# Kernel optimization log

Hardware: AMD Instinct MI355X
Metric: run time of the kernel (lower is better)

## Reference

```python
import jax, jax.numpy as jnp
import numpy as np
import math

B, D_MODEL, H, D_K, L = 24, 128, 8, 16, 512


def setup_inputs() -> dict:
    key = jax.random.key(0)
    ks = jax.random.split(key, 5)
    x = jax.random.normal(ks[0], (B, D_MODEL, L), dtype=jnp.float32)
    Wq = jax.random.normal(ks[1], (H, B, D_K, D_MODEL), dtype=jnp.float32)
    Wk = jax.random.normal(ks[2], (H, B, D_K, D_MODEL), dtype=jnp.float32)
    Wv = jax.random.normal(ks[3], (H, B, D_K, D_MODEL), dtype=jnp.float32)
    Wo = jax.random.normal(ks[4], (B, H * D_K, D_MODEL), dtype=jnp.float32)
    return {"x": x, "Wq": Wq, "Wk": Wk, "Wv": Wv, "Wo": Wo}


def reference(x, Wq, Wk, Wv, Wo):
    # Per-head, per-batch projections: [h,b,k,d] @ [b,d,l] -> [h,b,k,l]
    Q = jnp.einsum('hbkd,bdl->hbkl', Wq, x)
    K = jnp.einsum('hbkd,bdl->hbkl', Wk, x)
    V = jnp.einsum('hbkd,bdl->hbkl', Wv, x)
    # scores[h,b,l,m] = Q[:, :, :, l] . K[:, :, :, m]; torch softmax dim=1 of
    # the [B, L, L] score -> softmax over the QUERY axis l (axis=2 here).
    scores = jnp.einsum('hbkl,hbkm->hblm', Q, K) / math.sqrt(D_K)
    attn = jax.nn.softmax(scores, axis=2)
    # head_i = V @ attn : [h,b,v,l] @ [h,b,l,m] -> [h,b,v,m]
    heads = jnp.einsum('hbvl,hblm->hbvm', V, attn)
    # concat heads along channel dim: [b, h*v, L]
    head = heads.transpose(1, 0, 2, 3).reshape(B, H * D_K, L)
    # out = Wo @ head : [b, h*v, d_model] treated as [b,128,128] @ [b,128,L]
    out = jnp.einsum('bod,bdl->bol', Wo, head)
    return out
```

## Files before the change

### kernel.cpp

```cpp
#include <hip/hip_runtime.h>
#include <math.h>

#define NB 24
#define DM 128
#define NH 8
#define DK 16
#define LL 512
#define HB (NH * NB)

#define XTH_OFF 0
#define XTL_OFF 3145728
#define WHI_OFF 6291456
#define WLO_OFF 8650752
#define WOB_OFF 11010048
#define QB_OFF  11796480
#define KB_OFF  18087936
#define VB_OFF  24379392
#define HT_OFF  27525120

typedef __attribute__((ext_vector_type(8))) short bf16x8;
typedef __attribute__((ext_vector_type(4))) float f32x4;
typedef __attribute__((ext_vector_type(4))) int   i32x4;

#define MFMA  __builtin_amdgcn_mfma_f32_16x16x32_bf16
#define EXP2  __builtin_amdgcn_exp2f
#define BPERM __builtin_amdgcn_ds_bpermute

static __device__ __forceinline__ unsigned bfr(float x) {
    return (__float_as_uint(x) + 0x8000u) & 0xffff0000u;
}
static __device__ __forceinline__ unsigned pk2(unsigned e, unsigned o) {
    return (e >> 16) | o;
}

__global__ __launch_bounds__(256)
void prep(const float* __restrict__ x,
          const float* __restrict__ Wq,
          const float* __restrict__ Wk,
          const float* __restrict__ Wv,
          const float* __restrict__ Wo,
          unsigned short* __restrict__ xthi,
          unsigned short* __restrict__ xtlo,
          unsigned short* __restrict__ whi,
          unsigned short* __restrict__ wlo,
          unsigned short* __restrict__ wob)
{
    __shared__ float T[128][65];
    const int bid = blockIdx.x, tid = threadIdx.x;

    if (bid < 192) {
        const int b = bid >> 3, lc = bid & 7;
        const float* __restrict__ xb = x + (size_t)b * 65536 + lc * 64;
        #pragma unroll
        for (int i = 0; i < 32; ++i) {
            const int idx = i * 256 + tid;
            T[idx >> 6][idx & 63] = xb[(size_t)(idx >> 6) * LL + (idx & 63)];
        }
        __syncthreads();
        #pragma unroll
        for (int i = 0; i < 32; ++i) {
            const int idx = i * 256 + tid;
            const int l = idx >> 7, d = idx & 127;
            const float v = T[d][l];
            const unsigned h = bfr(v);
            const size_t o = (size_t)b * 65536 + (size_t)(lc * 64 + l) * DM + d;
            xthi[o] = (unsigned short)(h >> 16);
            xtlo[o] = (unsigned short)(bfr(v - __uint_as_float(h)) >> 16);
        }
    } else if (bid < 768) {
        const int w = bid - 192, hb = w / 3, mat = w - hb * 3;
        const float* __restrict__ src =
            (mat == 0 ? Wq : (mat == 1 ? Wk : Wv)) + (size_t)hb * 2048;
        unsigned short* __restrict__ dh = whi + (size_t)w * 2048;
        unsigned short* __restrict__ dl = wlo + (size_t)w * 2048;
        for (int i = tid; i < 2048; i += 256) {
            const float v = src[i];
            const unsigned h = bfr(v);
            dh[i] = (unsigned short)(h >> 16);
            dl[i] = (unsigned short)(bfr(v - __uint_as_float(h)) >> 16);
        }
    } else {
        const int w = bid - 768;
        const float* __restrict__ src = Wo + (size_t)w * 4096;
        unsigned short* __restrict__ d = wob + (size_t)w * 4096;
        for (int i = tid; i < 4096; i += 256)
            d[i] = (unsigned short)(bfr(src[i]) >> 16);
    }
}

__global__ __launch_bounds__(256)
void qkv_mfma(const unsigned short* __restrict__ xthi,
              const unsigned short* __restrict__ xtlo,
              const unsigned short* __restrict__ whi,
              const unsigned short* __restrict__ wlo,
              unsigned short* __restrict__ qb,
              unsigned short* __restrict__ kb,
              unsigned short* __restrict__ vb)
{
    const int blk  = blockIdx.x;
    const int nc   = blk & 1;
    const int hm   = blk >> 1;
    const int mat  = hm % 3;
    const int hb   = hm / 3;
    const int b    = hb % NB;
    const int wv   = threadIdx.x >> 6;
    const int lane = threadIdx.x & 63;
    const int g = lane >> 4, mR = lane & 15;
    const int l0 = nc * 256 + wv * 64;

    const unsigned short* __restrict__ wA = whi + (size_t)hm * 2048 + mR * 128 + g * 8;
    const unsigned short* __restrict__ wB = wlo + (size_t)hm * 2048 + mR * 128 + g * 8;
    const unsigned short* __restrict__ xh = xthi + (size_t)b * 65536 + g * 8;
    const unsigned short* __restrict__ xl = xtlo + (size_t)b * 65536 + g * 8;

    f32x4 C[4];
    #pragma unroll
    for (int t = 0; t < 4; ++t) C[t] = (f32x4){0.f, 0.f, 0.f, 0.f};

    #pragma unroll
    for (int kk = 0; kk < 4; ++kk) {
        const bf16x8 aH = *(const bf16x8*)(wA + kk * 32);
        const bf16x8 aL = *(const bf16x8*)(wB + kk * 32);
        #pragma unroll
        for (int t = 0; t < 4; ++t) {
            const size_t lo_ = (size_t)(l0 + t * 16 + mR) * DM + kk * 32;
            const bf16x8 bH = *(const bf16x8*)(xh + lo_);
            const bf16x8 bL = *(const bf16x8*)(xl + lo_);
            C[t] = MFMA(aH, bH, C[t], 0, 0, 0);
            C[t] = MFMA(aH, bL, C[t], 0, 0, 0);
            C[t] = MFMA(aL, bH, C[t], 0, 0, 0);
        }
    }

    if (mat == 2) {
        unsigned short* __restrict__ vo = vb + (size_t)hb * 8192;
        #pragma unroll
        for (int t = 0; t < 4; ++t) {
            const int l = l0 + t * 16 + mR;
            #pragma unroll
            for (int i = 0; i < 4; ++i)
                vo[(size_t)(4 * g + i) * LL + l] =
                    (unsigned short)(bfr(C[t][i]) >> 16);
        }
    } else {
        const float scale = (mat == 1) ? (0.25f * 1.44269504f) : 1.0f;
        unsigned short* __restrict__ dst =
            (mat == 0 ? qb : kb) + (size_t)hb * LL * 32;
        #pragma unroll
        for (int t = 0; t < 4; ++t) {
            const int l = l0 + t * 16 + mR;
            ushort4 hi4, lo4;
            #pragma unroll
            for (int i = 0; i < 4; ++i) {
                const float v = C[t][i] * scale;
                const unsigned h = bfr(v);
                const unsigned lw = bfr(v - __uint_as_float(h));
                ((unsigned short*)&hi4)[i] = (unsigned short)(h >> 16);
                ((unsigned short*)&lo4)[i] = (unsigned short)(lw >> 16);
            }
            *(ushort4*)(dst + (size_t)l * 32 + 4 * g)      = hi4;
            *(ushort4*)(dst + (size_t)l * 32 + 16 + 4 * g) = lo4;
        }
    }
}

static __device__ __forceinline__ void soft_pv(
    const f32x4& s0, const f32x4& s1, float tm, float& bar, float& sm,
    f32x4& O, const bf16x8& aV, int aLo, int aHi, bool up)
{
    const float nb = fmaxf(bar, tm + 32.f);
    const float f  = EXP2(bar - nb);
    bar = nb;
    const unsigned u0 = bfr(EXP2(s0[0]-nb)), u1 = bfr(EXP2(s0[1]-nb));
    const unsigned u2 = bfr(EXP2(s0[2]-nb)), u3 = bfr(EXP2(s0[3]-nb));
    const unsigned w0 = bfr(EXP2(s1[0]-nb)), w1 = bfr(EXP2(s1[1]-nb));
    const unsigned w2 = bfr(EXP2(s1[2]-nb)), w3 = bfr(EXP2(s1[3]-nb));
    const float sacc =
        ((__uint_as_float(u0) + __uint_as_float(u1)) +
         (__uint_as_float(u2) + __uint_as_float(u3))) +
        ((__uint_as_float(w0) + __uint_as_float(w1)) +
         (__uint_as_float(w2) + __uint_as_float(w3)));
    sm = fmaf(sm, f, sacc);
    O *= f;
    const int c0 = (int)pk2(u0, u1), c1 = (int)pk2(u2, u3);
    const int c2 = (int)pk2(w0, w1), c3 = (int)pk2(w2, w3);
    const int p00 = BPERM(aLo, c0), p02 = BPERM(aLo, c2);
    const int p10 = BPERM(aLo, c1), p12 = BPERM(aLo, c3);
    const int p20 = BPERM(aHi, c0), p22 = BPERM(aHi, c2);
    const int p30 = BPERM(aHi, c1), p32 = BPERM(aHi, c3);
    i32x4 bi = { up ? p00 : p02, up ? p10 : p12,
                 up ? p20 : p22, up ? p30 : p32 };
    O = MFMA(aV, __builtin_bit_cast(bf16x8, bi), O, 0, 0, 0);
}

__global__ __launch_bounds__(256)
void attn_mfma(const unsigned short* __restrict__ qb,
               const unsigned short* __restrict__ kb,
               const unsigned short* __restrict__ vb,
               unsigned short* __restrict__ ht)
{
    const int hb   = blockIdx.x >> 2;
    const int mc   = blockIdx.x & 3;
    const int tid  = threadIdx.x;
    const int wave = tid >> 6;
    const int lane = tid & 63;
    const int g    = lane >> 4;
    const int mR   = lane & 15;
    const int mb   = mc * 128 + wave * 32;

    const unsigned short* Kr0 = kb + ((size_t)hb * LL + mb + mR) * 32;
    const unsigned short* Kr1 = Kr0 + 16 * 32;
    const bf16x8 bK0  = *(const bf16x8*)(Kr0 + g * 8);
    const bf16x8 bK0s = *(const bf16x8*)(Kr0 + (g ^ 2) * 8);
    const bf16x8 bK1  = *(const bf16x8*)(Kr1 + g * 8);
    const bf16x8 bK1s = *(const bf16x8*)(Kr1 + (g ^ 2) * 8);

    const unsigned short* qrow = qb + ((size_t)hb * LL + mR) * 32 + g * 8;
    const unsigned short* vrow = vb + ((size_t)hb * DK + mR) * LL + g * 8;

    f32x4 O0 = {0.f,0.f,0.f,0.f}, O1 = {0.f,0.f,0.f,0.f};
    float bar0 = -1e30f, bar1 = -1e30f, sm0 = 0.f, sm1 = 0.f;

    const int aLo = ((g & 1) * 32 + mR) * 4;
    const int aHi = aLo + 64;
    const bool up = (g < 2);

    for (int l = 0; l < LL; l += 32) {
        const bf16x8 aQ0 = *(const bf16x8*)(qrow + (size_t)l * 32);
        const bf16x8 aQ1 = *(const bf16x8*)(qrow + (size_t)(l + 16) * 32);

        const f32x4 z = {0.f,0.f,0.f,0.f};
        f32x4 sA0 = MFMA(aQ0, bK0, z, 0,0,0);  sA0 = MFMA(aQ0, bK0s, sA0, 0,0,0);
        f32x4 sB0 = MFMA(aQ0, bK1, z, 0,0,0);  sB0 = MFMA(aQ0, bK1s, sB0, 0,0,0);
        f32x4 sA1 = MFMA(aQ1, bK0, z, 0,0,0);  sA1 = MFMA(aQ1, bK0s, sA1, 0,0,0);
        f32x4 sB1 = MFMA(aQ1, bK1, z, 0,0,0);  sB1 = MFMA(aQ1, bK1s, sB1, 0,0,0);

        float tmA = fmaxf(fmaxf(fmaxf(sA0[0],sA0[1]), fmaxf(sA0[2],sA0[3])),
                          fmaxf(fmaxf(sA1[0],sA1[1]), fmaxf(sA1[2],sA1[3])));
        float tmB = fmaxf(fmaxf(fmaxf(sB0[0],sB0[1]), fmaxf(sB0[2],sB0[3])),
                          fmaxf(fmaxf(sB1[0],sB1[1]), fmaxf(sB1[2],sB1[3])));
        tmA = fmaxf(tmA, __shfl_xor(tmA, 16, 64));
        tmA = fmaxf(tmA, __shfl_xor(tmA, 32, 64));
        tmB = fmaxf(tmB, __shfl_xor(tmB, 16, 64));
        tmB = fmaxf(tmB, __shfl_xor(tmB, 32, 64));

        if (__any(tmA + 64.f > bar0) || __any(tmB + 64.f > bar1)) {
            const bf16x8 aV = *(const bf16x8*)(vrow + l);
            soft_pv(sA0, sA1, tmA, bar0, sm0, O0, aV, aLo, aHi, up);
            soft_pv(sB0, sB1, tmB, bar1, sm1, O1, aV, aLo, aHi, up);
        }
    }

    sm0 += __shfl_xor(sm0, 16, 64);  sm0 += __shfl_xor(sm0, 32, 64);
    sm1 += __shfl_xor(sm1, 16, 64);  sm1 += __shfl_xor(sm1, 32, 64);
    const float i0 = 1.f / sm0, i1 = 1.f / sm1;

    const int h = hb / NB, bb = hb % NB;
    unsigned short* __restrict__ ho =
        ht + (size_t)bb * 65536 + (size_t)(mb + mR) * DM + h * 16 + 4 * g;
    ushort4 p0, p1;
    #pragma unroll
    for (int i = 0; i < 4; ++i) {
        ((unsigned short*)&p0)[i] = (unsigned short)(bfr(O0[i] * i0) >> 16);
        ((unsigned short*)&p1)[i] = (unsigned short)(bfr(O1[i] * i1) >> 16);
    }
    *(ushort4*)ho              = p0;
    *(ushort4*)(ho + 16 * DM)  = p1;
}

__global__ __launch_bounds__(256)
void out_mfma(const unsigned short* __restrict__ wob,
              const unsigned short* __restrict__ ht,
              float* __restrict__ out)
{
    const int blk  = blockIdx.x;
    const int b    = blk >> 5;
    const int mq   = (blk >> 4) & 1;
    const int nq   = blk & 15;
    const int wv   = threadIdx.x >> 6;
    const int lane = threadIdx.x & 63;
    const int g = lane >> 4, mR = lane & 15;
    const int m0 = (mq * 4 + wv) * 16;
    const int n0 = nq * 32;

    const unsigned short* __restrict__ A =
        wob + (size_t)b * 16384 + (size_t)(m0 + mR) * DM + g * 8;
    const unsigned short* __restrict__ B = ht + (size_t)b * 65536 + g * 8;

    f32x4 C0 = {0.f,0.f,0.f,0.f}, C1 = {0.f,0.f,0.f,0.f};
    #pragma unroll
    for (int kk = 0; kk < 4; ++kk) {
        const bf16x8 aW = *(const bf16x8*)(A + kk * 32);
        const bf16x8 b0 = *(const bf16x8*)(B + (size_t)(n0 + mR) * DM + kk * 32);
        const bf16x8 b1 = *(const bf16x8*)(B + (size_t)(n0 + 16 + mR) * DM + kk * 32);
        C0 = MFMA(aW, b0, C0, 0, 0, 0);
        C1 = MFMA(aW, b1, C1, 0, 0, 0);
    }

    float* __restrict__ ob = out + (size_t)b * 65536 + (size_t)(m0 + 4 * g) * LL;
    #pragma unroll
    for (int i = 0; i < 4; ++i) {
        ob[(size_t)i * LL + n0 + mR]      = C0[i];
        ob[(size_t)i * LL + n0 + 16 + mR] = C1[i];
    }
}

extern "C" void kernel_launch(void* const* d_in, const int* in_sizes, int n_in,
                              void* d_out, int out_size, void* d_ws, size_t ws_size,
                              hipStream_t stream) {
    const float* x  = (const float*)d_in[0];
    const float* Wq = (const float*)d_in[1];
    const float* Wk = (const float*)d_in[2];
    const float* Wv = (const float*)d_in[3];
    const float* Wo = (const float*)d_in[4];
    float* out = (float*)d_out;

    char* ws = (char*)d_ws;
    unsigned short* xthi = (unsigned short*)(ws + XTH_OFF);
    unsigned short* xtlo = (unsigned short*)(ws + XTL_OFF);
    unsigned short* whi  = (unsigned short*)(ws + WHI_OFF);
    unsigned short* wlo  = (unsigned short*)(ws + WLO_OFF);
    unsigned short* wob  = (unsigned short*)(ws + WOB_OFF);
    unsigned short* qb   = (unsigned short*)(ws + QB_OFF);
    unsigned short* kb   = (unsigned short*)(ws + KB_OFF);
    unsigned short* vb   = (unsigned short*)(ws + VB_OFF);
    unsigned short* ht   = (unsigned short*)(ws + HT_OFF);

    prep     <<<864,     256, 0, stream>>>(x, Wq, Wk, Wv, Wo, xthi, xtlo, whi, wlo, wob);
    qkv_mfma <<<HB * 6,  256, 0, stream>>>(xthi, xtlo, whi, wlo, qb, kb, vb);
    attn_mfma<<<HB * 4,  256, 0, stream>>>(qb, kb, vb, ht);
    out_mfma <<<NB * 32, 256, 0, stream>>>(wob, ht, out);
}
```

Before: 127.3 us.

## Fuse Q/K/V projections per block, pack bf16 stores, use hardware bf16 convert

The QKV kernel now computes all three projections in one block, so the x tiles loaded per k-step are reused across Q, K and V instead of being reloaded by three separate blocks. The grid shrinks from six to four blocks per head-batch. The prep kernel writes bf16 pairs as 32-bit stores and uses a smaller shared tile. The attention softmax uses v_cvt_pk_bf16_f32 for packing, and soft_pv is skipped independently for each half when its max check does not trigger. Fewer blocks and more accumulators per thread may lower occupancy and latency hiding.

After: 116.7 us. 1.09x faster.

```diff
diff --git a/kernel.cpp b/kernel.cpp
--- a/kernel.cpp
+++ b/kernel.cpp
@@ -29,8 +29,11 @@
 static __device__ __forceinline__ unsigned bfr(float x) {
     return (__float_as_uint(x) + 0x8000u) & 0xffff0000u;
 }
-static __device__ __forceinline__ unsigned pk2(unsigned e, unsigned o) {
-    return (e >> 16) | o;
+
+static __device__ __forceinline__ unsigned cvtpk(float a, float b) {
+    unsigned r;
+    asm("v_cvt_pk_bf16_f32 %0, %1, %2" : "=v"(r) : "v"(a), "v"(b));
+    return r;
 }
 
 __global__ __launch_bounds__(256)
@@ -45,27 +48,36 @@
           unsigned short* __restrict__ wlo,
           unsigned short* __restrict__ wob)
 {
-    __shared__ float T[128][65];
+    __shared__ float T[64][65];
     const int bid = blockIdx.x, tid = threadIdx.x;
 
     if (bid < 192) {
         const int b = bid >> 3, lc = bid & 7;
-        const float* __restrict__ xb = x + (size_t)b * 65536 + lc * 64;
-        #pragma unroll
-        for (int i = 0; i < 32; ++i) {
-            const int idx = i * 256 + tid;
-            T[idx >> 6][idx & 63] = xb[(size_t)(idx >> 6) * LL + (idx & 63)];
-        }
-        __syncthreads();
-        #pragma unroll
-        for (int i = 0; i < 32; ++i) {
-            const int idx = i * 256 + tid;
-            const int l = idx >> 7, d = idx & 127;
-            const float v = T[d][l];
-            const unsigned h = bfr(v);
-            const size_t o = (size_t)b * 65536 + (size_t)(lc * 64 + l) * DM + d;
-            xthi[o] = (unsigned short)(h >> 16);
-            xtlo[o] = (unsigned short)(bfr(v - __uint_as_float(h)) >> 16);
+        #pragma unroll
+        for (int half = 0; half < 2; ++half) {
+            const int d0 = half << 6;
+            const float* __restrict__ xb =
+                x + (size_t)b * 65536 + (size_t)d0 * LL + lc * 64;
+            if (half) __syncthreads();
+            #pragma unroll
+            for (int i = 0; i < 16; ++i) {
+                const int idx = i * 256 + tid;
+                T[idx >> 6][idx & 63] = xb[(size_t)(idx >> 6) * LL + (idx & 63)];
+            }
+            __syncthreads();
+            #pragma unroll
+            for (int i = 0; i < 8; ++i) {
+                const int idx = (i * 256 + tid) * 2;
+                const int l = idx >> 6, dd = idx & 63;
+                const float v0 = T[dd][l], v1 = T[dd + 1][l];
+                const unsigned h0 = bfr(v0), h1 = bfr(v1);
+                const unsigned e0 = bfr(v0 - __uint_as_float(h0));
+                const unsigned e1 = bfr(v1 - __uint_as_float(h1));
+                const size_t o = (size_t)b * 65536 +
+                                 (size_t)(lc * 64 + l) * DM + d0 + dd;
+                *(unsigned*)(xthi + o) = (h0 >> 16) | (h1 & 0xffff0000u);
+                *(unsigned*)(xtlo + o) = (e0 >> 16) | (e1 & 0xffff0000u);
+            }
         }
     } else if (bid < 768) {
         const int w = bid - 192, hb = w / 3, mat = w - hb * 3;
@@ -73,18 +85,22 @@
             (mat == 0 ? Wq : (mat == 1 ? Wk : Wv)) + (size_t)hb * 2048;
         unsigned short* __restrict__ dh = whi + (size_t)w * 2048;
         unsigned short* __restrict__ dl = wlo + (size_t)w * 2048;
-        for (int i = tid; i < 2048; i += 256) {
-            const float v = src[i];
-            const unsigned h = bfr(v);
-            dh[i] = (unsigned short)(h >> 16);
-            dl[i] = (unsigned short)(bfr(v - __uint_as_float(h)) >> 16);
+        for (int i = tid; i < 1024; i += 256) {
+            const float v0 = src[2 * i], v1 = src[2 * i + 1];
+            const unsigned h0 = bfr(v0), h1 = bfr(v1);
+            const unsigned e0 = bfr(v0 - __uint_as_float(h0));
+            const unsigned e1 = bfr(v1 - __uint_as_float(h1));
+            *(unsigned*)(dh + 2 * i) = (h0 >> 16) | (h1 & 0xffff0000u);
+            *(unsigned*)(dl + 2 * i) = (e0 >> 16) | (e1 & 0xffff0000u);
         }
     } else {
         const int w = bid - 768;
         const float* __restrict__ src = Wo + (size_t)w * 4096;
         unsigned short* __restrict__ d = wob + (size_t)w * 4096;
-        for (int i = tid; i < 4096; i += 256)
-            d[i] = (unsigned short)(bfr(src[i]) >> 16);
+        for (int i = tid; i < 2048; i += 256) {
+            const float v0 = src[2 * i], v1 = src[2 * i + 1];
+            *(unsigned*)(d + 2 * i) = (bfr(v0) >> 16) | (bfr(v1) & 0xffff0000u);
+        }
     }
 }
 
@@ -98,61 +114,72 @@
               unsigned short* __restrict__ vb)
 {
     const int blk  = blockIdx.x;
-    const int nc   = blk & 1;
-    const int hm   = blk >> 1;
-    const int mat  = hm % 3;
-    const int hb   = hm / 3;
+    const int nc   = blk & 3;
+    const int hb   = blk >> 2;
     const int b    = hb % NB;
     const int wv   = threadIdx.x >> 6;
     const int lane = threadIdx.x & 63;
     const int g = lane >> 4, mR = lane & 15;
-    const int l0 = nc * 256 + wv * 64;
-
-    const unsigned short* __restrict__ wA = whi + (size_t)hm * 2048 + mR * 128 + g * 8;
-    const unsigned short* __restrict__ wB = wlo + (size_t)hm * 2048 + mR * 128 + g * 8;
+    const int l0 = nc * 128 + wv * 32;
+
+    const unsigned short* __restrict__ wAh =
+        whi + (size_t)hb * 6144 + mR * 128 + g * 8;
+    const unsigned short* __restrict__ wAl =
+        wlo + (size_t)hb * 6144 + mR * 128 + g * 8;
     const unsigned short* __restrict__ xh = xthi + (size_t)b * 65536 + g * 8;
     const unsigned short* __restrict__ xl = xtlo + (size_t)b * 65536 + g * 8;
 
-    f32x4 C[4];
-    #pragma unroll
-    for (int t = 0; t < 4; ++t) C[t] = (f32x4){0.f, 0.f, 0.f, 0.f};
+    f32x4 C[3][2];
+    #pragma unroll
+    for (int m = 0; m < 3; ++m)
+        #pragma unroll
+        for (int t = 0; t < 2; ++t) C[m][t] = (f32x4){0.f, 0.f, 0.f, 0.f};
 
     #pragma unroll
     for (int kk = 0; kk < 4; ++kk) {
-        const bf16x8 aH = *(const bf16x8*)(wA + kk * 32);
-        const bf16x8 aL = *(const bf16x8*)(wB + kk * 32);
-        #pragma unroll
-        for (int t = 0; t < 4; ++t) {
+        bf16x8 bH[2], bL[2];
+        #pragma unroll
+        for (int t = 0; t < 2; ++t) {
             const size_t lo_ = (size_t)(l0 + t * 16 + mR) * DM + kk * 32;
-            const bf16x8 bH = *(const bf16x8*)(xh + lo_);
-            const bf16x8 bL = *(const bf16x8*)(xl + lo_);
-            C[t] = MFMA(aH, bH, C[t], 0, 0, 0);
-            C[t] = MFMA(aH, bL, C[t], 0, 0, 0);
-            C[t] = MFMA(aL, bH, C[t], 0, 0, 0);
-        }
-    }
-
-    if (mat == 2) {
+            bH[t] = *(const bf16x8*)(xh + lo_);
+            bL[t] = *(const bf16x8*)(xl + lo_);
+        }
+        #pragma unroll
+        for (int m = 0; m < 3; ++m) {
+            const bf16x8 aH = *(const bf16x8*)(wAh + m * 2048 + kk * 32);
+            const bf16x8 aL = *(const bf16x8*)(wAl + m * 2048 + kk * 32);
+            #pragma unroll
+            for (int t = 0; t < 2; ++t) {
+                C[m][t] = MFMA(aH, bH[t], C[m][t], 0, 0, 0);
+                C[m][t] = MFMA(aH, bL[t], C[m][t], 0, 0, 0);
+                C[m][t] = MFMA(aL, bH[t], C[m][t], 0, 0, 0);
+            }
+        }
+    }
+
+    {
         unsigned short* __restrict__ vo = vb + (size_t)hb * 8192;
         #pragma unroll
-        for (int t = 0; t < 4; ++t) {
+        for (int t = 0; t < 2; ++t) {
             const int l = l0 + t * 16 + mR;
             #pragma unroll
             for (int i = 0; i < 4; ++i)
                 vo[(size_t)(4 * g + i) * LL + l] =
-                    (unsigned short)(bfr(C[t][i]) >> 16);
-        }
-    } else {
-        const float scale = (mat == 1) ? (0.25f * 1.44269504f) : 1.0f;
+                    (unsigned short)(bfr(C[2][t][i]) >> 16);
+        }
+    }
+    #pragma unroll
+    for (int m = 0; m < 2; ++m) {
+        const float scale = m ? (0.25f * 1.44269504f) : 1.0f;
         unsigned short* __restrict__ dst =
-            (mat == 0 ? qb : kb) + (size_t)hb * LL * 32;
-        #pragma unroll
-        for (int t = 0; t < 4; ++t) {
+            (m ? kb : qb) + (size_t)hb * LL * 32;
+        #pragma unroll
+        for (int t = 0; t < 2; ++t) {
             const int l = l0 + t * 16 + mR;
             ushort4 hi4, lo4;
             #pragma unroll
             for (int i = 0; i < 4; ++i) {
-                const float v = C[t][i] * scale;
+                const float v = C[m][t][i] * scale;
                 const unsigned h = bfr(v);
                 const unsigned lw = bfr(v - __uint_as_float(h));
                 ((unsigned short*)&hi4)[i] = (unsigned short)(h >> 16);
@@ -171,23 +198,21 @@
     const float nb = fmaxf(bar, tm + 32.f);
     const float f  = EXP2(bar - nb);
     bar = nb;
-    const unsigned u0 = bfr(EXP2(s0[0]-nb)), u1 = bfr(EXP2(s0[1]-nb));
-    const unsigned u2 = bfr(EXP2(s0[2]-nb)), u3 = bfr(EXP2(s0[3]-nb));
-    const unsigned w0 = bfr(EXP2(s1[0]-nb)), w1 = bfr(EXP2(s1[1]-nb));
-    const unsigned w2 = bfr(EXP2(s1[2]-nb)), w3 = bfr(EXP2(s1[3]-nb));
+    const unsigned c0 = cvtpk(EXP2(s0[0] - nb), EXP2(s0[1] - nb));
+    const unsigned c1 = cvtpk(EXP2(s0[2] - nb), EXP2(s0[3] - nb));
+    const unsigned c2 = cvtpk(EXP2(s1[0] - nb), EXP2(s1[1] - nb));
+    const unsigned c3 = cvtpk(EXP2(s1[2] - nb), EXP2(s1[3] - nb));
     const float sacc =
-        ((__uint_as_float(u0) + __uint_as_float(u1)) +
-         (__uint_as_float(u2) + __uint_as_float(u3))) +
-        ((__uint_as_float(w0) + __uint_as_float(w1)) +
-         (__uint_as_float(w2) + __uint_as_float(w3)));
+        ((__uint_as_float(c0 << 16) + __uint_as_float(c0 & 0xffff0000u)) +
+         (__uint_as_float(c1 << 16) + __uint_as_float(c1 & 0xffff0000u))) +
+        ((__uint_as_float(c2 << 16) + __uint_as_float(c2 & 0xffff0000u)) +
+         (__uint_as_float(c3 << 16) + __uint_as_float(c3 & 0xffff0000u)));
     sm = fmaf(sm, f, sacc);
     O *= f;
-    const int c0 = (int)pk2(u0, u1), c1 = (int)pk2(u2, u3);
-    const int c2 = (int)pk2(w0, w1), c3 = (int)pk2(w2, w3);
-    const int p00 = BPERM(aLo, c0), p02 = BPERM(aLo, c2);
-    const int p10 = BPERM(aLo, c1), p12 = BPERM(aLo, c3);
-    const int p20 = BPERM(aHi, c0), p22 = BPERM(aHi, c2);
-    const int p30 = BPERM(aHi, c1), p32 = BPERM(aHi, c3);
+    const int p00 = BPERM(aLo, (int)c0), p02 = BPERM(aLo, (int)c2);
+    const int p10 = BPERM(aLo, (int)c1), p12 = BPERM(aLo, (int)c3);
+    const int p20 = BPERM(aHi, (int)c0), p22 = BPERM(aHi, (int)c2);
+    const int p30 = BPERM(aHi, (int)c1), p32 = BPERM(aHi, (int)c3);
     i32x4 bi = { up ? p00 : p02, up ? p10 : p12,
                  up ? p20 : p22, up ? p30 : p32 };
     O = MFMA(aV, __builtin_bit_cast(bf16x8, bi), O, 0, 0, 0);
@@ -244,10 +269,12 @@
         tmB = fmaxf(tmB, __shfl_xor(tmB, 16, 64));
         tmB = fmaxf(tmB, __shfl_xor(tmB, 32, 64));
 
-        if (__any(tmA + 64.f > bar0) || __any(tmB + 64.f > bar1)) {
+        const bool pA = __any(tmA + 64.f > bar0);
+        const bool pB = __any(tmB + 64.f > bar1);
+        if (pA || pB) {
             const bf16x8 aV = *(const bf16x8*)(vrow + l);
-            soft_pv(sA0, sA1, tmA, bar0, sm0, O0, aV, aLo, aHi, up);
-            soft_pv(sB0, sB1, tmB, bar1, sm1, O1, aV, aLo, aHi, up);
+            if (pA) soft_pv(sA0, sA1, tmA, bar0, sm0, O0, aV, aLo, aHi, up);
+            if (pB) soft_pv(sB0, sB1, tmB, bar1, sm1, O1, aV, aLo, aHi, up);
         }
     }
 
@@ -327,7 +354,7 @@
     unsigned short* ht   = (unsigned short*)(ws + HT_OFF);
 
     prep     <<<864,     256, 0, stream>>>(x, Wq, Wk, Wv, Wo, xthi, xtlo, whi, wlo, wob);
-    qkv_mfma <<<HB * 6,  256, 0, stream>>>(xthi, xtlo, whi, wlo, qb, kb, vb);
+    qkv_mfma <<<HB * 4,  256, 0, stream>>>(xthi, xtlo, whi, wlo, qb, kb, vb);
     attn_mfma<<<HB * 4,  256, 0, stream>>>(qb, kb, vb, ht);
     out_mfma <<<NB * 32, 256, 0, stream>>>(wob, ht, out);
 }
```
